# Optimization experiments

Hardware: AMD Instinct MI355X
Metric: run time of the kernel (lower is better)

## Reference

```python
import jax, jax.numpy as jnp
import numpy as np

B, C, H, W = 2, 256, 32, 32
PK, CK = 256, 256


def setup_inputs() -> dict:
    key = jax.random.key(0)
    ks = jax.random.split(key, 9)
    s = 1.0 / np.sqrt(C)
    return {
        'x': jax.random.normal(ks[0], (B, C, H, W), jnp.float32),
        'primary_indices': jax.random.randint(ks[1], (B, PK), 0, B * H * W),
        'compare_indices': jax.random.randint(ks[2], (B, CK), 0, B * H * W),
        'pre_w': jax.random.uniform(ks[3], (3, C, C), jnp.float32, -s, s),
        'pre_b': jax.random.uniform(ks[4], (3, C), jnp.float32, -s, s),
        'post_w': jax.random.uniform(ks[5], (2, C, C), jnp.float32, -s, s),
        'post_b': jax.random.uniform(ks[6], (2, C), jnp.float32, -s, s),
        'post_out_w': jax.random.uniform(ks[7], (2, C), jnp.float32, -s, s),
        'post_out_b': jax.random.uniform(ks[8], (2,), jnp.float32, -s, s),
    }


def reference(x, primary_indices, compare_indices, pre_w, pre_b,
              post_w, post_b, post_out_w, post_out_b):
    # pre_compare: stack of 1x1 convs (c->c->c->c), ReLU between layers
    h = x
    for i in range(3):
        h = jnp.einsum('bchw,oc->bohw', h, pre_w[i]) + pre_b[i][None, :, None, None]
        if i < 2:
            h = jax.nn.relu(h)
    bs, c, hh, ww = h.shape
    # flatten to [bs*h*w, c] node features (matches torch transpose+reshape)
    flat = h.reshape(bs, c, hh * ww).transpose(0, 2, 1).reshape(bs * hh * ww, c)
    # gather primary / compare node features with global flat indices
    xp = flat[primary_indices.reshape(-1)].reshape(bs, -1, c).transpose(0, 2, 1)  # [b,c,pk]
    xc = flat[compare_indices.reshape(-1)].reshape(bs, -1, c).transpose(0, 2, 1)  # [b,c,ck]
    # broadcast pairwise squared difference -> [b,c,pk,ck]
    xx = (xp[:, :, :, None] - xc[:, :, None, :]) ** 2
    # post_compare: 1x1 conv stack c->c->c->2, ReLU between layers
    g = xx
    for i in range(2):
        g = jax.nn.relu(jnp.einsum('bcpq,oc->bopq', g, post_w[i]) + post_b[i][None, :, None, None])
    out = jnp.einsum('bcpq,oc->bopq', g, post_out_w) + post_out_b[None, :, None, None]
    return out  # [b, 2, pk, ck]
```

## Files before the change

### kernel.cpp

```cpp
#include <hip/hip_runtime.h>

typedef unsigned short u16;
typedef short bf16x8 __attribute__((ext_vector_type(8)));
typedef float f32x4 __attribute__((ext_vector_type(4)));
typedef u16 u16x4 __attribute__((ext_vector_type(4)));

__device__ __forceinline__ float b2f(u16 h) {
  unsigned u = ((unsigned)h) << 16;
  return __builtin_bit_cast(float, u);
}
__device__ __forceinline__ u16 f2b(float f) {
  return __builtin_bit_cast(u16, (__bf16)f);
}
__device__ __forceinline__ void gld_lds16(const void* g, void* l) {
  __builtin_amdgcn_global_load_lds(
      (__attribute__((address_space(1))) void*)(g),
      (__attribute__((address_space(3))) void*)(l), 16, 0, 0);
}

__global__ void dense_edge_prep(const float* __restrict__ x,
                                const float* __restrict__ pre_w,
                                const float* __restrict__ post_w,
                                u16* __restrict__ wb, u16* __restrict__ xt) {
  const int blk = blockIdx.x;
  const int t = threadIdx.x;
  if (blk < 160) {
    const int id = blk * 256 + t;
    const int layer = id >> 13;
    const int sid = id & 8191;
    const int m = sid >> 5;
    const int s8 = sid & 31;
    const float* src = (layer < 2) ? (post_w + layer * 65536)
                                   : (pre_w + (layer - 2) * 65536);
    u16* dst = wb + layer * 65536;
    f32x4 a = *(const f32x4*)(src + m * 256 + s8 * 8);
    f32x4 c = *(const f32x4*)(src + m * 256 + s8 * 8 + 4);
    bf16x8 o;
#pragma unroll
    for (int j = 0; j < 4; j++) o[j] = (short)f2b(a[j]);
#pragma unroll
    for (int j = 0; j < 4; j++) o[4 + j] = (short)f2b(c[j]);
    *(bf16x8*)(dst + (s8 * 256 + m) * 8) = o;
  } else {
    __shared__ float tile[32 * 65];
    const int xb = blk - 160;
    const int b = xb >> 7;
    const int ct = (xb >> 4) & 7;
    const int ht = xb & 15;
    const int c0 = ct * 32, hw0 = ht * 64;
#pragma unroll
    for (int rep = 0; rep < 8; rep++) {
      const int idx = rep * 256 + t;
      const int cl = idx >> 6, hl = idx & 63;
      tile[cl * 65 + hl] = x[(b * 256 + c0 + cl) * 1024 + hw0 + hl];
    }
    __syncthreads();
    const int hl = t >> 2, c8 = t & 3;
    bf16x8 o;
#pragma unroll
    for (int i = 0; i < 8; i++) o[i] = (short)f2b(tile[(c8 * 8 + i) * 65 + hl]);
    *(bf16x8*)(xt + (b * 1024 + hw0 + hl) * 256 + c0 + c8 * 8) = o;
  }
}

__global__ __launch_bounds__(256, 2) void dense_edge_pre(
    const u16* __restrict__ xt, const u16* __restrict__ wpre,
    const float* __restrict__ preb, u16* __restrict__ flat) {
  __shared__ u16 feat[2][4096];
  const int t = threadIdx.x;
  const int wv = t >> 6, ln = t & 63;
  const int nb = blockIdx.x * 16;
  const int q4 = ln >> 4, r15 = ln & 15;

#pragma unroll
  for (int i = 0; i < 2; i++) {
    const int slot = wv * 128 + i * 64 + ln;
    const int s8 = slot >> 4, nl = slot & 15;
    gld_lds16(xt + (nb + nl) * 256 + s8 * 8, &feat[0][slot * 8]);
  }
  __syncthreads();

#pragma unroll
  for (int l = 0; l < 3; l++) {
    const u16* wl = wpre + l * 65536;
    f32x4 acc[4];
    f32x4 zero = {0.f, 0.f, 0.f, 0.f};
#pragma unroll
    for (int mt = 0; mt < 4; mt++) acc[mt] = zero;
#pragma unroll
    for (int s = 0; s < 8; s++) {
      bf16x8 bv = *(const bf16x8*)(&feat[l & 1][((s * 4 + q4) * 16 + r15) * 8]);
#pragma unroll
      for (int mt = 0; mt < 4; mt++) {
        bf16x8 av = *(const bf16x8*)(wl + ((s * 4 + q4) * 256 + wv * 64 + mt * 16 + r15) * 8);
        acc[mt] = __builtin_amdgcn_mfma_f32_16x16x32_bf16(av, bv, acc[mt], 0, 0, 0);
      }
    }
    if (l < 2) {
#pragma unroll
      for (int mt = 0; mt < 4; mt++) {
        const int o = wv * 64 + mt * 16 + q4 * 4;
        f32x4 bb = *(const f32x4*)(preb + l * 256 + o);
        u16x4 pk;
#pragma unroll
        for (int r = 0; r < 4; r++) {
          float v = fmaxf(acc[mt][r] + bb[r], 0.f);
          pk[r] = f2b(v);
        }
        *(u16x4*)(&feat[(l + 1) & 1][((o >> 3) * 16 + r15) * 8 + (o & 7)]) = pk;
      }
      __syncthreads();
    } else {
#pragma unroll
      for (int mt = 0; mt < 4; mt++) {
        const int o = wv * 64 + mt * 16 + q4 * 4;
        f32x4 bb = *(const f32x4*)(preb + 512 + o);
        u16x4 pk;
#pragma unroll
        for (int r = 0; r < 4; r++) pk[r] = f2b(acc[mt][r] + bb[r]);
        *(u16x4*)(flat + (nb + r15) * 256 + o) = pk;
      }
    }
  }
}

#define NT 8
__global__ __launch_bounds__(512, 2) void dense_edge_main(
    const u16* __restrict__ flat, const int* __restrict__ pidx,
    const int* __restrict__ cidx, const u16* __restrict__ w1s,
    const u16* __restrict__ w2s, const float* __restrict__ b1,
    const float* __restrict__ b2, const float* __restrict__ w3,
    const float* __restrict__ b3, float* __restrict__ out) {
  __shared__ u16 xxbuf[2][16384];
  __shared__ u16 t1buf[2][16384];
  __shared__ u16 pstage[2048];
  __shared__ u16 qstage[2][2048];
  __shared__ float pbuf[2][8][2][64];

  const int t = threadIdx.x;
  const int wv = t >> 6;
  const int ln = t & 63;
  const int q4 = ln >> 4, r15 = ln & 15;
  const int blk = blockIdx.x;
  const int tile0 = blk * NT;
  const int b = tile0 >> 10;
  const int pt = (tile0 >> 5) & 31;
  const int qt0 = tile0 & 31;
  const int p0 = pt * 8;

  bf16x8 w1f[2][8], w2f[2][8];
#pragma unroll
  for (int s = 0; s < 8; s++)
#pragma unroll
    for (int mt = 0; mt < 2; mt++) {
      const int off = ((s * 4 + q4) * 256 + wv * 32 + mt * 16 + r15) * 8;
      w1f[mt][s] = *(const bf16x8*)(w1s + off);
      w2f[mt][s] = *(const bf16x8*)(w2s + off);
    }

  const int slot4 = (wv & 3) * 64 + ln;
  const int srow = slot4 & 7, scc = slot4 >> 3;
  if (wv < 4) {
    const int pn = pidx[b * 256 + p0 + srow];
    gld_lds16(flat + pn * 256 + scc * 8, &pstage[slot4 * 8]);
  } else {
    const int qn = cidx[b * 256 + qt0 * 8 + srow];
    gld_lds16(flat + qn * 256 + scc * 8, &qstage[0][slot4 * 8]);
  }
  int qn_pro = 0, qn_cur = 0;
  if (wv >= 4) {
    qn_pro = cidx[b * 256 + (qt0 + 1) * 8 + srow];
    qn_cur = cidx[b * 256 + (qt0 + 2) * 8 + srow];
  }
  __syncthreads();

  const int prow = ln >> 3, qrow = ln & 7;

  bf16x8 pa[4];
#pragma unroll
  for (int i = 0; i < 4; i++)
    pa[i] = *(const bf16x8*)(&pstage[((wv * 4 + i) * 8 + prow) * 8]);

  auto do_xx = [&](int jx) {
    const u16* qs = qstage[jx & 1];
    u16* xb = xxbuf[jx & 1];
#pragma unroll
    for (int i = 0; i < 4; i++) {
      const int cc = wv * 4 + i;
      bf16x8 av = pa[i];
      bf16x8 bv = *(const bf16x8*)(&qs[(cc * 8 + qrow) * 8]);
      bf16x8 ov;
#pragma unroll
      for (int jj = 0; jj < 8; jj++) {
        float d = b2f((u16)av[jj]) - b2f((u16)bv[jj]);
        ov[jj] = (short)f2b(d * d);
      }
      *(bf16x8*)(&xb[(cc * 64 + ln) * 8]) = ov;
    }
  };

  auto do_g1 = [&](int jg) {
    const u16* xb = xxbuf[jg & 1];
    f32x4 acc[2][4];
    {
      f32x4 zero = {0.f, 0.f, 0.f, 0.f};
#pragma unroll
      for (int mt = 0; mt < 2; mt++)
#pragma unroll
        for (int nt = 0; nt < 4; nt++) acc[mt][nt] = zero;
    }
    __builtin_amdgcn_s_setprio(1);
#pragma unroll
    for (int s = 0; s < 8; s++) {
      bf16x8 bfr[4];
#pragma unroll
      for (int nt = 0; nt < 4; nt++)
        bfr[nt] = *(const bf16x8*)(xb + ((s * 4 + q4) * 64 + nt * 16 + r15) * 8);
#pragma unroll
      for (int mt = 0; mt < 2; mt++)
#pragma unroll
        for (int nt = 0; nt < 4; nt++)
          acc[mt][nt] = __builtin_amdgcn_mfma_f32_16x16x32_bf16(w1f[mt][s], bfr[nt], acc[mt][nt], 0, 0, 0);
    }
    __builtin_amdgcn_s_setprio(0);
#pragma unroll
    for (int mt = 0; mt < 2; mt++) {
      const int o = wv * 32 + mt * 16 + q4 * 4;
      f32x4 bb = *(const f32x4*)(b1 + o);
#pragma unroll
      for (int nt = 0; nt < 4; nt++) {
        const int nn = nt * 16 + r15;
        u16x4 pk;
#pragma unroll
        for (int r = 0; r < 4; r++) {
          float v = fmaxf(acc[mt][nt][r] + bb[r], 0.f);
          pk[r] = f2b(v);
        }
        *(u16x4*)(&t1buf[jg & 1][((o >> 3) * 64 + nn) * 8 + (o & 7)]) = pk;
      }
    }
  };

  auto do_g2 = [&](int jg) {
    const u16* tb = t1buf[jg & 1];
    f32x4 acc[2][4];
    {
      f32x4 zero = {0.f, 0.f, 0.f, 0.f};
#pragma unroll
      for (int mt = 0; mt < 2; mt++)
#pragma unroll
        for (int nt = 0; nt < 4; nt++) acc[mt][nt] = zero;
    }
    __builtin_amdgcn_s_setprio(1);
#pragma unroll
    for (int s = 0; s < 8; s++) {
      bf16x8 bfr[4];
#pragma unroll
      for (int nt = 0; nt < 4; nt++)
        bfr[nt] = *(const bf16x8*)(tb + ((s * 4 + q4) * 64 + nt * 16 + r15) * 8);
#pragma unroll
      for (int mt = 0; mt < 2; mt++)
#pragma unroll
        for (int nt = 0; nt < 4; nt++)
          acc[mt][nt] = __builtin_amdgcn_mfma_f32_16x16x32_bf16(w2f[mt][s], bfr[nt], acc[mt][nt], 0, 0, 0);
    }
    __builtin_amdgcn_s_setprio(0);
    float part[2][4] = {{0.f, 0.f, 0.f, 0.f}, {0.f, 0.f, 0.f, 0.f}};
#pragma unroll
    for (int mt = 0; mt < 2; mt++) {
      const int o = wv * 32 + mt * 16 + q4 * 4;
      f32x4 bb = *(const f32x4*)(b2 + o);
      f32x4 w3a = *(const f32x4*)(w3 + o);
      f32x4 w3b = *(const f32x4*)(w3 + 256 + o);
#pragma unroll
      for (int nt = 0; nt < 4; nt++) {
#pragma unroll
        for (int r = 0; r < 4; r++) {
          float v = fmaxf(acc[mt][nt][r] + bb[r], 0.f);
          part[0][nt] += v * w3a[r];
          part[1][nt] += v * w3b[r];
        }
      }
    }
#pragma unroll
    for (int o3 = 0; o3 < 2; o3++)
#pragma unroll
      for (int nt = 0; nt < 4; nt++) {
        part[o3][nt] += __shfl_xor(part[o3][nt], 16, 64);
        part[o3][nt] += __shfl_xor(part[o3][nt], 32, 64);
      }
    if (q4 == 0) {
#pragma unroll
      for (int o3 = 0; o3 < 2; o3++)
#pragma unroll
        for (int nt = 0; nt < 4; nt++)
          pbuf[jg & 1][wv][o3][nt * 16 + r15] = part[o3][nt];
    }
  };

  do_xx(0);
  if (wv >= 4) gld_lds16(flat + qn_pro * 256 + scc * 8, &qstage[1][slot4 * 8]);
  __syncthreads();

#pragma unroll 1
  for (int j = 0; j <= NT; j++) {
    if (j >= 2 && t < 128) {
      const int jo = j - 2;
      const int o3 = t >> 6;
      const int n = t & 63;
      float v = b3[o3];
#pragma unroll
      for (int k = 0; k < 8; k++) v += pbuf[jo & 1][k][o3][n];
      out[((b * 2 + o3) * 256 + p0 + (n >> 3)) * 256 + (qt0 + jo) * 8 + (n & 7)] = v;
    }
    if (j < NT - 2 && wv >= 4) {
      gld_lds16(flat + qn_cur * 256 + scc * 8, &qstage[j & 1][slot4 * 8]);
      if (j < NT - 3) qn_cur = cidx[b * 256 + (qt0 + j + 3) * 8 + srow];
    }
    if (wv & 1) {
      if (j < NT - 1) do_xx(j + 1);
      if (j > 0) do_g2(j - 1);
      if (j < NT) do_g1(j);
    } else {
      if (j < NT) do_g1(j);
      if (j > 0) do_g2(j - 1);
      if (j < NT - 1) do_xx(j + 1);
    }
    __syncthreads();
  }

  if (t < 128) {
    const int jo = NT - 1;
    const int o3 = t >> 6;
    const int n = t & 63;
    float v = b3[o3];
#pragma unroll
    for (int k = 0; k < 8; k++) v += pbuf[jo & 1][k][o3][n];
    out[((b * 2 + o3) * 256 + p0 + (n >> 3)) * 256 + (qt0 + jo) * 8 + (n & 7)] = v;
  }
}

extern "C" void kernel_launch(void* const* d_in, const int* in_sizes, int n_in,
                              void* d_out, int out_size, void* d_ws, size_t ws_size,
                              hipStream_t stream) {
  (void)in_sizes; (void)n_in; (void)out_size; (void)ws_size;
  const float* x          = (const float*)d_in[0];
  const int*   pidx       = (const int*)d_in[1];
  const int*   cidx       = (const int*)d_in[2];
  const float* pre_w      = (const float*)d_in[3];
  const float* pre_b      = (const float*)d_in[4];
  const float* post_w     = (const float*)d_in[5];
  const float* post_b     = (const float*)d_in[6];
  const float* post_out_w = (const float*)d_in[7];
  const float* post_out_b = (const float*)d_in[8];
  float* out = (float*)d_out;

  u16* ws   = (u16*)d_ws;
  u16* wb   = ws;
  u16* w1s  = wb;
  u16* w2s  = wb + 65536;
  u16* wpre = wb + 131072;
  u16* xt   = ws + 327680;
  u16* flat = ws + 851968;

  dense_edge_prep<<<416, 256, 0, stream>>>(x, pre_w, post_w, wb, xt);
  dense_edge_pre<<<128, 256, 0, stream>>>(xt, wpre, pre_b, flat);
  dense_edge_main<<<256, 512, 0, stream>>>(flat, pidx, cidx, w1s, w2s,
                                           post_b, post_b + 256,
                                           post_out_w, post_out_b, out);
}
```

Baseline: 117.2 us.

## Fuse prep, pre-MLP and main kernels into one cooperative launch with grid sync

Merges the three kernels into a single cooperative kernel. The first 128 blocks transpose x, convert it to bf16 and run the three pre-compare layers into a flat buffer. A grid-wide sync then separates that phase from the pairwise main stage. Weights are converted from fp32 to bf16 in registers as they are loaded, which removes the separate prep pass and its workspace round trip. This saves two launch gaps and intermediate global traffic, but adds grid-sync overhead and leaves half the grid idle during the pre phase.

```diff
diff --git a/kernel.cpp b/kernel.cpp
--- a/kernel.cpp
+++ b/kernel.cpp
@@ -1,4 +1,6 @@
 #include <hip/hip_runtime.h>
+#include <hip/hip_cooperative_groups.h>
+namespace cg = cooperative_groups;
 
 typedef unsigned short u16;
 typedef short bf16x8 __attribute__((ext_vector_type(8)));
@@ -18,123 +20,18 @@
       (__attribute__((address_space(3))) void*)(l), 16, 0, 0);
 }
 
-__global__ void dense_edge_prep(const float* __restrict__ x,
-                                const float* __restrict__ pre_w,
-                                const float* __restrict__ post_w,
-                                u16* __restrict__ wb, u16* __restrict__ xt) {
-  const int blk = blockIdx.x;
-  const int t = threadIdx.x;
-  if (blk < 160) {
-    const int id = blk * 256 + t;
-    const int layer = id >> 13;
-    const int sid = id & 8191;
-    const int m = sid >> 5;
-    const int s8 = sid & 31;
-    const float* src = (layer < 2) ? (post_w + layer * 65536)
-                                   : (pre_w + (layer - 2) * 65536);
-    u16* dst = wb + layer * 65536;
-    f32x4 a = *(const f32x4*)(src + m * 256 + s8 * 8);
-    f32x4 c = *(const f32x4*)(src + m * 256 + s8 * 8 + 4);
-    bf16x8 o;
-#pragma unroll
-    for (int j = 0; j < 4; j++) o[j] = (short)f2b(a[j]);
-#pragma unroll
-    for (int j = 0; j < 4; j++) o[4 + j] = (short)f2b(c[j]);
-    *(bf16x8*)(dst + (s8 * 256 + m) * 8) = o;
-  } else {
-    __shared__ float tile[32 * 65];
-    const int xb = blk - 160;
-    const int b = xb >> 7;
-    const int ct = (xb >> 4) & 7;
-    const int ht = xb & 15;
-    const int c0 = ct * 32, hw0 = ht * 64;
-#pragma unroll
-    for (int rep = 0; rep < 8; rep++) {
-      const int idx = rep * 256 + t;
-      const int cl = idx >> 6, hl = idx & 63;
-      tile[cl * 65 + hl] = x[(b * 256 + c0 + cl) * 1024 + hw0 + hl];
-    }
-    __syncthreads();
-    const int hl = t >> 2, c8 = t & 3;
-    bf16x8 o;
-#pragma unroll
-    for (int i = 0; i < 8; i++) o[i] = (short)f2b(tile[(c8 * 8 + i) * 65 + hl]);
-    *(bf16x8*)(xt + (b * 1024 + hw0 + hl) * 256 + c0 + c8 * 8) = o;
-  }
-}
-
-__global__ __launch_bounds__(256, 2) void dense_edge_pre(
-    const u16* __restrict__ xt, const u16* __restrict__ wpre,
-    const float* __restrict__ preb, u16* __restrict__ flat) {
-  __shared__ u16 feat[2][4096];
-  const int t = threadIdx.x;
-  const int wv = t >> 6, ln = t & 63;
-  const int nb = blockIdx.x * 16;
-  const int q4 = ln >> 4, r15 = ln & 15;
-
-#pragma unroll
-  for (int i = 0; i < 2; i++) {
-    const int slot = wv * 128 + i * 64 + ln;
-    const int s8 = slot >> 4, nl = slot & 15;
-    gld_lds16(xt + (nb + nl) * 256 + s8 * 8, &feat[0][slot * 8]);
-  }
-  __syncthreads();
-
-#pragma unroll
-  for (int l = 0; l < 3; l++) {
-    const u16* wl = wpre + l * 65536;
-    f32x4 acc[4];
-    f32x4 zero = {0.f, 0.f, 0.f, 0.f};
-#pragma unroll
-    for (int mt = 0; mt < 4; mt++) acc[mt] = zero;
-#pragma unroll
-    for (int s = 0; s < 8; s++) {
-      bf16x8 bv = *(const bf16x8*)(&feat[l & 1][((s * 4 + q4) * 16 + r15) * 8]);
-#pragma unroll
-      for (int mt = 0; mt < 4; mt++) {
-        bf16x8 av = *(const bf16x8*)(wl + ((s * 4 + q4) * 256 + wv * 64 + mt * 16 + r15) * 8);
-        acc[mt] = __builtin_amdgcn_mfma_f32_16x16x32_bf16(av, bv, acc[mt], 0, 0, 0);
-      }
-    }
-    if (l < 2) {
-#pragma unroll
-      for (int mt = 0; mt < 4; mt++) {
-        const int o = wv * 64 + mt * 16 + q4 * 4;
-        f32x4 bb = *(const f32x4*)(preb + l * 256 + o);
-        u16x4 pk;
-#pragma unroll
-        for (int r = 0; r < 4; r++) {
-          float v = fmaxf(acc[mt][r] + bb[r], 0.f);
-          pk[r] = f2b(v);
-        }
-        *(u16x4*)(&feat[(l + 1) & 1][((o >> 3) * 16 + r15) * 8 + (o & 7)]) = pk;
-      }
-      __syncthreads();
-    } else {
-#pragma unroll
-      for (int mt = 0; mt < 4; mt++) {
-        const int o = wv * 64 + mt * 16 + q4 * 4;
-        f32x4 bb = *(const f32x4*)(preb + 512 + o);
-        u16x4 pk;
-#pragma unroll
-        for (int r = 0; r < 4; r++) pk[r] = f2b(acc[mt][r] + bb[r]);
-        *(u16x4*)(flat + (nb + r15) * 256 + o) = pk;
-      }
-    }
-  }
-}
-
 #define NT 8
-__global__ __launch_bounds__(512, 2) void dense_edge_main(
-    const u16* __restrict__ flat, const int* __restrict__ pidx,
-    const int* __restrict__ cidx, const u16* __restrict__ w1s,
-    const u16* __restrict__ w2s, const float* __restrict__ b1,
-    const float* __restrict__ b2, const float* __restrict__ w3,
-    const float* __restrict__ b3, float* __restrict__ out) {
-  __shared__ u16 xxbuf[2][16384];
-  __shared__ u16 t1buf[2][16384];
-  __shared__ u16 pstage[2048];
-  __shared__ u16 qstage[2][2048];
+__global__ __launch_bounds__(512, 2) void dense_edge_all(
+    const float* __restrict__ x, const int* __restrict__ pidx,
+    const int* __restrict__ cidx, const float* __restrict__ pre_w,
+    const float* __restrict__ pre_b, const float* __restrict__ post_w,
+    const float* __restrict__ post_b, const float* __restrict__ post_out_w,
+    const float* __restrict__ post_out_b, u16* flat,
+    float* __restrict__ out) {
+  __shared__ __align__(16) u16 xxbuf[2][16384];
+  __shared__ __align__(16) u16 t1buf[2][16384];
+  __shared__ __align__(16) u16 pstage[2048];
+  __shared__ __align__(16) u16 qstage[2][2048];
   __shared__ float pbuf[2][8][2][64];
 
   const int t = threadIdx.x;
@@ -142,21 +39,130 @@
   const int ln = t & 63;
   const int q4 = ln >> 4, r15 = ln & 15;
   const int blk = blockIdx.x;
+
+  if (blk < 128) {
+    const int nb = blk * 16;
+    const int bA = nb >> 10, hw0 = nb & 1023;
+    float* tile = (float*)&xxbuf[0][0];
+    u16* feat0 = &t1buf[0][0];
+    u16* feat1 = &t1buf[0][4096];
+    {
+      const int c = t >> 1, half = t & 1;
+      const float* src = x + (bA * 256 + c) * 1024 + hw0 + half * 8;
+      f32x4 v0 = *(const f32x4*)src;
+      f32x4 v1 = *(const f32x4*)(src + 4);
+#pragma unroll
+      for (int e = 0; e < 4; e++) {
+        tile[(half * 8 + e) * 260 + c] = v0[e];
+        tile[(half * 8 + 4 + e) * 260 + c] = v1[e];
+      }
+    }
+    __syncthreads();
+    {
+      const float* p = tile + (t & 15) * 260 + (t >> 4) * 8;
+      f32x4 a = *(const f32x4*)p, c4 = *(const f32x4*)(p + 4);
+      bf16x8 o8;
+#pragma unroll
+      for (int k = 0; k < 4; k++) {
+        o8[k] = (short)f2b(a[k]);
+        o8[4 + k] = (short)f2b(c4[k]);
+      }
+      *(bf16x8*)(feat0 + t * 8) = o8;
+    }
+    __syncthreads();
+#pragma unroll 1
+    for (int l = 0; l < 3; l++) {
+      const float* wl = pre_w + l * 65536;
+      bf16x8 wreg[2][8];
+#pragma unroll
+      for (int s = 0; s < 8; s++)
+#pragma unroll
+        for (int mt = 0; mt < 2; mt++) {
+          const float* p = wl + (wv * 32 + mt * 16 + r15) * 256 + (s * 4 + q4) * 8;
+          f32x4 a = *(const f32x4*)p, c4 = *(const f32x4*)(p + 4);
+          bf16x8 o8;
+#pragma unroll
+          for (int k = 0; k < 4; k++) {
+            o8[k] = (short)f2b(a[k]);
+            o8[4 + k] = (short)f2b(c4[k]);
+          }
+          wreg[mt][s] = o8;
+        }
+      const u16* fin = (l & 1) ? feat1 : feat0;
+      u16* fout = (l & 1) ? feat0 : feat1;
+      f32x4 acc[2];
+      acc[0] = {0.f, 0.f, 0.f, 0.f};
+      acc[1] = {0.f, 0.f, 0.f, 0.f};
+#pragma unroll
+      for (int s = 0; s < 8; s++) {
+        bf16x8 bv = *(const bf16x8*)(fin + ((s * 4 + q4) * 16 + r15) * 8);
+#pragma unroll
+        for (int mt = 0; mt < 2; mt++)
+          acc[mt] = __builtin_amdgcn_mfma_f32_16x16x32_bf16(wreg[mt][s], bv, acc[mt], 0, 0, 0);
+      }
+      if (l < 2) {
+#pragma unroll
+        for (int mt = 0; mt < 2; mt++) {
+          const int o = wv * 32 + mt * 16 + q4 * 4;
+          f32x4 bb = *(const f32x4*)(pre_b + l * 256 + o);
+          u16x4 pk;
+#pragma unroll
+          for (int r = 0; r < 4; r++) {
+            float v = fmaxf(acc[mt][r] + bb[r], 0.f);
+            pk[r] = f2b(v);
+          }
+          *(u16x4*)(fout + ((o >> 3) * 16 + r15) * 8 + (o & 7)) = pk;
+        }
+        __syncthreads();
+      } else {
+#pragma unroll
+        for (int mt = 0; mt < 2; mt++) {
+          const int o = wv * 32 + mt * 16 + q4 * 4;
+          f32x4 bb = *(const f32x4*)(pre_b + 512 + o);
+          u16x4 pk;
+#pragma unroll
+          for (int r = 0; r < 4; r++) pk[r] = f2b(acc[mt][r] + bb[r]);
+          *(u16x4*)(flat + (nb + r15) * 256 + o) = pk;
+        }
+      }
+    }
+    __threadfence();
+  }
+
+  bf16x8 w1f[2][8], w2f[2][8];
+#pragma unroll
+  for (int s = 0; s < 8; s++)
+#pragma unroll
+    for (int mt = 0; mt < 2; mt++) {
+      const int o = wv * 32 + mt * 16 + r15, c0 = (s * 4 + q4) * 8;
+      const float* p1 = post_w + o * 256 + c0;
+      const float* p2 = post_w + 65536 + o * 256 + c0;
+      f32x4 a1 = *(const f32x4*)p1, d1 = *(const f32x4*)(p1 + 4);
+      f32x4 a2 = *(const f32x4*)p2, d2 = *(const f32x4*)(p2 + 4);
+      bf16x8 o1, o2;
+#pragma unroll
+      for (int k = 0; k < 4; k++) {
+        o1[k] = (short)f2b(a1[k]);
+        o1[4 + k] = (short)f2b(d1[k]);
+        o2[k] = (short)f2b(a2[k]);
+        o2[4 + k] = (short)f2b(d2[k]);
+      }
+      w1f[mt][s] = o1;
+      w2f[mt][s] = o2;
+    }
+
+  cg::this_grid().sync();
+
+  const float* b1 = post_b;
+  const float* b2 = post_b + 256;
+  const float* w3 = post_out_w;
+  const float* b3 = post_out_b;
+
   const int tile0 = blk * NT;
   const int b = tile0 >> 10;
   const int pt = (tile0 >> 5) & 31;
   const int qt0 = tile0 & 31;
   const int p0 = pt * 8;
-
-  bf16x8 w1f[2][8], w2f[2][8];
-#pragma unroll
-  for (int s = 0; s < 8; s++)
-#pragma unroll
-    for (int mt = 0; mt < 2; mt++) {
-      const int off = ((s * 4 + q4) * 256 + wv * 32 + mt * 16 + r15) * 8;
-      w1f[mt][s] = *(const bf16x8*)(w1s + off);
-      w2f[mt][s] = *(const bf16x8*)(w2s + off);
-    }
 
   const int slot4 = (wv & 3) * 64 + ln;
   const int srow = slot4 & 7, scc = slot4 >> 3;
@@ -354,18 +360,12 @@
   const float* post_out_w = (const float*)d_in[7];
   const float* post_out_b = (const float*)d_in[8];
   float* out = (float*)d_out;
-
-  u16* ws   = (u16*)d_ws;
-  u16* wb   = ws;
-  u16* w1s  = wb;
-  u16* w2s  = wb + 65536;
-  u16* wpre = wb + 131072;
-  u16* xt   = ws + 327680;
-  u16* flat = ws + 851968;
-
-  dense_edge_prep<<<416, 256, 0, stream>>>(x, pre_w, post_w, wb, xt);
-  dense_edge_pre<<<128, 256, 0, stream>>>(xt, wpre, pre_b, flat);
-  dense_edge_main<<<256, 512, 0, stream>>>(flat, pidx, cidx, w1s, w2s,
-                                           post_b, post_b + 256,
-                                           post_out_w, post_out_b, out);
-}
+  u16* flat = (u16*)d_ws;
+
+  void* args[] = {(void*)&x,         (void*)&pidx,       (void*)&cidx,
+                  (void*)&pre_w,     (void*)&pre_b,      (void*)&post_w,
+                  (void*)&post_b,    (void*)&post_out_w, (void*)&post_out_b,
+                  (void*)&flat,      (void*)&out};
+  hipLaunchCooperativeKernel((const void*)dense_edge_all, dim3(256), dim3(512),
+                             args, 0, stream);
+}
```

Result: slower. 221.0 us (+88.5%).
